# Performance work log

Measured on AMD Instinct MI355X. Metric: run time of the kernel, lower is better.

The kernel has to match this reference:

```python
import jax, jax.numpy as jnp
import numpy as np

B, N, D = 64, 128, 512
NEG = 1e30


def _gru_cell(x, h, Wi, Wh, bi, bh):
    # torch nn.GRUCell math
    gi = x @ Wi.T + bi  # (B, 3D)
    gh = h @ Wh.T + bh  # (B, 3D)
    ir, iz, inn = jnp.split(gi, 3, axis=-1)
    hr, hz, hn = jnp.split(gh, 3, axis=-1)
    r = jax.nn.sigmoid(ir + hr)
    z = jax.nn.sigmoid(iz + hz)
    n = jnp.tanh(inn + r * hn)
    return (1.0 - z) * n + z * h


def setup_inputs() -> dict:
    key = jax.random.key(0)
    ks = jax.random.split(key, 16)
    s = 1.0 / np.sqrt(D)
    u = lambda k, shape: jax.random.uniform(k, shape, jnp.float32, -s, s)
    adj = jax.random.randint(ks[13], (B, N, N), 0, 2, jnp.int32)
    adj = adj.at[:, :, 0].set(1)  # ensure each causal prefix has >=1 unmasked edge
    s_mask = jax.random.randint(ks[14], (B, N, N), 0, 2, jnp.int32)
    o_mask = 1 - s_mask
    return {
        "features": jax.random.normal(ks[0], (B, N, D), jnp.float32),
        "Wi_c": u(ks[1], (3 * D, D)),
        "Wh_c": u(ks[2], (3 * D, D)),
        "bi_c": u(ks[3], (3 * D,)),
        "bh_c": u(ks[4], (3 * D,)),
        "Wi_p": u(ks[5], (3 * D, D)),
        "Wh_p": u(ks[6], (3 * D, D)),
        "bi_p": u(ks[7], (3 * D,)),
        "bh_p": u(ks[8], (3 * D,)),
        "lin_w": u(ks[9], (1, 2 * D)),
        "lin_b": u(ks[10], (1,)),
        "Wr0": u(ks[11], (D, D)),
        "Wr1": u(ks[12], (D, D)),
        "adj": adj,
        "s_mask": s_mask,
        "o_mask": o_mask,
    }


def reference(features, Wi_c, Wh_c, bi_c, bh_c, Wi_p, Wh_p, bi_p, bh_p,
              lin_w, lin_b, Wr0, Wr1, adj, s_mask, o_mask):
    dt = features.dtype
    adj_f = adj.astype(dt)
    s_f = s_mask.astype(dt)
    o_f = o_mask.astype(dt)
    wq = lin_w[0, :D]   # applies to Q half of cat(Q, K)
    wk = lin_w[0, D:]   # applies to K half
    b = lin_b[0]
    pos = jnp.arange(N)

    # step 0
    x0 = features[:, 0]
    zeros = jnp.zeros((B, D), dt)
    C0 = _gru_cell(x0, zeros, Wi_c, Wh_c, bi_c, bh_c)
    P0 = _gru_cell(zeros, x0, Wi_p, Wh_p, bi_p, bh_p)
    H0 = jnp.zeros((B, N, D), dt).at[:, 0].set(C0 + P0)

    def step(H, inputs):
        i, x, adj_row, s_row, o_row = inputs
        # masked graph attention over the causal prefix [0, i)
        alpha = (x @ wq)[:, None] + H @ wk + b          # (B, N)
        valid = adj_row * (pos < i).astype(dt)          # (B, N)
        alpha = alpha - (1.0 - valid) * NEG
        w = jax.nn.softmax(alpha, axis=1)               # (B, N)
        V = (H @ Wr0.T) * s_row[:, :, None] + (H @ Wr1.T) * o_row[:, :, None]
        M = jnp.einsum('bn,bnd->bd', w, V)              # (B, D)
        C = _gru_cell(x, M, Wi_c, Wh_c, bi_c, bh_c)
        P = _gru_cell(M, x, Wi_p, Wh_p, bi_p, bh_p)
        H = H.at[:, i].set(C + P)
        return H, None

    xs = (jnp.arange(1, N),
          jnp.swapaxes(features, 0, 1)[1:],
          jnp.swapaxes(adj_f, 0, 1)[1:],
          jnp.swapaxes(s_f, 0, 1)[1:],
          jnp.swapaxes(o_f, 0, 1)[1:])
    H1, _ = jax.lax.scan(step, H0, xs)
    return H1
```

## Files before the change

kernel.cpp:

```cpp
#include <hip/hip_runtime.h>

#define BB 64
#define NN 128
#define DD 512
#define NBLK 128
#define NTHR 512
#define GCOLS 24
#define WCS 2056
#define WXS 1032
#define BCS 6656
#define UBE (BB * 2048)

typedef unsigned short u16;
typedef unsigned int u32;
typedef unsigned long long u64;
typedef __attribute__((ext_vector_type(8))) __bf16 bf16x8;
typedef __attribute__((ext_vector_type(4))) float f32x4;

#define MFMA16(a, b, c) __builtin_amdgcn_mfma_f32_16x16x32_bf16((a), (b), (c), 0, 0, 0)

__device__ __forceinline__ float b2f(u16 u) {
    union { u32 i; float f; } c; c.i = ((u32)u) << 16; return c.f;
}
__device__ __forceinline__ u16 f2b(float f) {
    union { float f; u32 i; } c; c.f = f;
    return (u16)((c.i + 0x7FFFu + ((c.i >> 16) & 1u)) >> 16);
}
__device__ __forceinline__ float sigm(float x) { return 1.f / (1.f + __expf(-x)); }
__device__ __forceinline__ float tanh_(float x) {
    x = fminf(fmaxf(x, -15.f), 15.f);
    float e = __expf(2.f * x);
    return (e - 1.f) / (e + 1.f);
}

__device__ __forceinline__ float ld_cohf(const float* p) {
    return __hip_atomic_load((float*)p, __ATOMIC_RELAXED, __HIP_MEMORY_SCOPE_AGENT);
}
__device__ __forceinline__ void st_cohf(float* p, float v) {
    __hip_atomic_store(p, v, __ATOMIC_RELAXED, __HIP_MEMORY_SCOPE_AGENT);
}
__device__ __forceinline__ void st_cohu32(u32* p, u32 v) {
    __hip_atomic_store(p, v, __ATOMIC_RELAXED, __HIP_MEMORY_SCOPE_AGENT);
}

template<bool CACHED>
__device__ __forceinline__ bf16x8 ldu16(const u16* p) {
    if constexpr (CACHED) {
        return *(const bf16x8*)p;
    } else {
        union { bf16x8 v; u64 q[2]; } u;
        u.q[0] = __hip_atomic_load((u64*)p,     __ATOMIC_RELAXED, __HIP_MEMORY_SCOPE_AGENT);
        u.q[1] = __hip_atomic_load((u64*)p + 1, __ATOMIC_RELAXED, __HIP_MEMORY_SCOPE_AGENT);
        return u.v;
    }
}

__device__ __forceinline__ void gbar(int* sync, int gen, int blk) {
    __syncthreads();
    int* epoch = sync;
    if (blk == 0) {
        const int t = threadIdx.x;
        int done = (t == 0 || t >= NBLK) ? 1 : 0;
        int* myarr = sync + 256 + t * 16;
        int it = 0;
        for (;;) {
            if (!done) {
                int v = ((it & 15) == 15)
                    ? __hip_atomic_load(myarr, __ATOMIC_ACQUIRE, __HIP_MEMORY_SCOPE_AGENT)
                    : __hip_atomic_load(myarr, __ATOMIC_RELAXED, __HIP_MEMORY_SCOPE_AGENT);
                done = (v >= gen);
            }
            ++it;
            if (__syncthreads_and(done)) break;
            __builtin_amdgcn_s_sleep(1);
        }
        if (t == 0) {
            (void)__hip_atomic_load(sync + 256 + 16, __ATOMIC_ACQUIRE, __HIP_MEMORY_SCOPE_AGENT);
            __hip_atomic_store(epoch, gen, __ATOMIC_RELEASE, __HIP_MEMORY_SCOPE_AGENT);
        }
        __syncthreads();
    } else {
        if (threadIdx.x == 0) {
            __hip_atomic_store(sync + 256 + blk * 16, gen, __ATOMIC_RELEASE, __HIP_MEMORY_SCOPE_AGENT);
            int it = 0;
            for (;;) {
                int v = ((it & 15) == 15)
                    ? __hip_atomic_load(epoch, __ATOMIC_ACQUIRE, __HIP_MEMORY_SCOPE_AGENT)
                    : __hip_atomic_load(epoch, __ATOMIC_RELAXED, __HIP_MEMORY_SCOPE_AGENT);
                ++it;
                if (v >= gen) break;
                __builtin_amdgcn_s_sleep(1);
            }
            (void)__hip_atomic_load(epoch, __ATOMIC_ACQUIRE, __HIP_MEMORY_SCOPE_AGENT);
        }
        __syncthreads();
    }
}

__device__ __forceinline__ void gbar_lite(int* flags, int gen, int blk,
                                          int nsig, bool sig, bool wait) {
    __syncthreads();
    if (sig && threadIdx.x == 0)
        __hip_atomic_store(flags + blk * 32, gen, __ATOMIC_RELAXED, __HIP_MEMORY_SCOPE_AGENT);
    if (wait) {
        const int t = threadIdx.x;
        int done = (t >= nsig) ? 1 : 0;
        int* f = flags + t * 32;
        for (;;) {
            if (!done) {
                int v = __hip_atomic_load(f, __ATOMIC_RELAXED, __HIP_MEMORY_SCOPE_AGENT);
                done = (v >= gen);
            }
            if (__syncthreads_and(done)) break;
            __builtin_amdgcn_s_sleep(2);
        }
    }
    asm volatile("" ::: "memory");
    __builtin_amdgcn_sched_barrier(0);
}

template<bool CACHED>
__device__ __forceinline__ void gates_merged(
    const u16* __restrict__ ub, const u16* s_wc, const float* s_gb,
    float* __restrict__ bc, int blk, int rt, int lr, int lq)
{
    const int cc0 = lr, cc1 = lr + 8;
    const u16* w0 = s_wc + cc0 * WCS;
    const u16* w1 = s_wc + cc1 * WCS;
    const u16* arow = ub + (size_t)(rt * 16 + lr) * 2048;
    f32x4 acc0 = {0.f, 0.f, 0.f, 0.f}, acc1 = {0.f, 0.f, 0.f, 0.f};
    #pragma unroll 4
    for (int c = 0; c < 16; ++c) {
        int kk = c * 32 + lq * 8;
        bf16x8 ah = ldu16<CACHED>(arow + kk);
        bf16x8 al = ldu16<CACHED>(arow + 512 + kk);
        bf16x8 wh0 = *(const bf16x8*)(w0 + kk);
        bf16x8 wl0 = *(const bf16x8*)(w0 + 1024 + kk);
        bf16x8 wh1 = *(const bf16x8*)(w1 + kk);
        bf16x8 wl1 = *(const bf16x8*)(w1 + 1024 + kk);
        acc0 = MFMA16(ah, wh0, acc0); acc0 = MFMA16(al, wh0, acc0); acc0 = MFMA16(ah, wl0, acc0);
        acc1 = MFMA16(ah, wh1, acc1); acc1 = MFMA16(al, wh1, acc1); acc1 = MFMA16(ah, wl1, acc1);
    }
    #pragma unroll 4
    for (int c = 0; c < 16; ++c) {
        int kk = c * 32 + lq * 8;
        bf16x8 ah = ldu16<CACHED>(arow + 1024 + kk);
        bf16x8 al = ldu16<CACHED>(arow + 1536 + kk);
        bf16x8 wh0 = *(const bf16x8*)(w0 + 512 + kk);
        bf16x8 wl0 = *(const bf16x8*)(w0 + 1536 + kk);
        bf16x8 wh1 = *(const bf16x8*)(w1 + 512 + kk);
        bf16x8 wl1 = *(const bf16x8*)(w1 + 1536 + kk);
        acc0 = MFMA16(ah, wh0, acc0); acc0 = MFMA16(al, wh0, acc0); acc0 = MFMA16(ah, wl0, acc0);
        acc1 = MFMA16(ah, wh1, acc1); acc1 = MFMA16(al, wh1, acc1); acc1 = MFMA16(ah, wl1, acc1);
    }
    float b0 = s_gb[cc0], b1 = s_gb[cc1];
    int col0 = blk * GCOLS + cc0, col1 = blk * GCOLS + cc1;
    #pragma unroll
    for (int r = 0; r < 4; ++r) {
        size_t row = (size_t)(rt * 16 + lq * 4 + r) * BCS;
        st_cohf(bc + row + 512 + col0, acc0[r] + b0);
        st_cohf(bc + row + 512 + col1, acc1[r] + b1);
    }
}

__device__ __forceinline__ void x_task(
    int i, const u16* __restrict__ featblob, const u16* s_wxw, const float* s_xb,
    float* __restrict__ bc, int blk, int task, int lr, int lq)
{
    const int ct = task & 1, rt = task >> 1;
    const int cc = ct * 8 + lr;
    const int col = blk * GCOLS + cc;
    const u16* wcol = s_wxw + cc * WXS;
    const u16* arow = featblob + (size_t)(i * 64 + rt * 16 + lr) * 1024;
    f32x4 acc = {0.f, 0.f, 0.f, 0.f};
    #pragma unroll 4
    for (int c = 0; c < 16; ++c) {
        int kk = c * 32 + lq * 8;
        bf16x8 ah = *(const bf16x8*)(arow + kk);
        bf16x8 al = *(const bf16x8*)(arow + 512 + kk);
        bf16x8 wh = *(const bf16x8*)(wcol + kk);
        bf16x8 wl = *(const bf16x8*)(wcol + 512 + kk);
        acc = MFMA16(ah, wh, acc); acc = MFMA16(al, wh, acc); acc = MFMA16(ah, wl, acc);
    }
    float bias = s_xb[cc];
    #pragma unroll
    for (int r = 0; r < 4; ++r)
        st_cohf(bc + (size_t)(rt * 16 + lq * 4 + r) * BCS + 3584 + col, acc[r] + bias);
}

template<bool CACHED>
__device__ __forceinline__ void m_task(
    const u16* __restrict__ ub, const u16* __restrict__ WrB,
    float* __restrict__ bc, int blk, int lr, int lq)
{
    const int ct = blk >> 2, rt = blk & 3;
    const int col = ct * 16 + lr;
    const u16* wcol = WrB + (size_t)col * 2048;
    const u16* arow = ub + (size_t)(rt * 16 + lr) * 2048;
    f32x4 acc = {0.f, 0.f, 0.f, 0.f};
    #pragma unroll 4
    for (int c = 0; c < 16; ++c) {
        int kk = c * 32 + lq * 8;
        bf16x8 a0h = ldu16<CACHED>(arow + kk);
        bf16x8 a0l = ldu16<CACHED>(arow + 512 + kk);
        bf16x8 a1h = ldu16<CACHED>(arow + 1024 + kk);
        bf16x8 a1l = ldu16<CACHED>(arow + 1536 + kk);
        bf16x8 w0h = *(const bf16x8*)(wcol + kk);
        bf16x8 w0l = *(const bf16x8*)(wcol + 512 + kk);
        bf16x8 w1h = *(const bf16x8*)(wcol + 1024 + kk);
        bf16x8 w1l = *(const bf16x8*)(wcol + 1536 + kk);
        acc = MFMA16(a0h, w0h, acc); acc = MFMA16(a0l, w0h, acc); acc = MFMA16(a0h, w0l, acc);
        acc = MFMA16(a1h, w1h, acc); acc = MFMA16(a1l, w1h, acc); acc = MFMA16(a1h, w1l, acc);
    }
    #pragma unroll
    for (int r = 0; r < 4; ++r)
        st_cohf(bc + (size_t)(rt * 16 + lq * 4 + r) * BCS + col, acc[r]);
}

template<bool CACHED>
__device__ __forceinline__ void phb(
    int i, const u16* __restrict__ ub, const u16* __restrict__ featblob,
    const u16* __restrict__ WrB, const u16* s_wc, const u16* s_wxw,
    const float* s_gb, const float* s_xb,
    float* __restrict__ bc, int blk, int wv, int lr, int lq)
{
    if (wv < 4) {
        gates_merged<CACHED>(ub, s_wc, s_gb, bc, blk, wv, lr, lq);
    } else if (wv == 4) {
        x_task(i, featblob, s_wxw, s_xb, bc, blk, 0, lr, lq);
        x_task(i, featblob, s_wxw, s_xb, bc, blk, 1, lr, lq);
        x_task(i, featblob, s_wxw, s_xb, bc, blk, 2, lr, lq);
    } else if (wv == 5) {
        x_task(i, featblob, s_wxw, s_xb, bc, blk, 3, lr, lq);
        x_task(i, featblob, s_wxw, s_xb, bc, blk, 4, lr, lq);
        x_task(i, featblob, s_wxw, s_xb, bc, blk, 5, lr, lq);
    } else if (wv == 6) {
        x_task(i, featblob, s_wxw, s_xb, bc, blk, 6, lr, lq);
        x_task(i, featblob, s_wxw, s_xb, bc, blk, 7, lr, lq);
    } else {
        m_task<CACHED>(ub, WrB, bc, blk, lr, lq);
    }
}

__global__ __launch_bounds__(NTHR) void grn_kernel(
    const float* __restrict__ feat, const float* __restrict__ Wi_c, const float* __restrict__ Wh_c,
    const float* __restrict__ bi_c, const float* __restrict__ bh_c,
    const float* __restrict__ Wi_p, const float* __restrict__ Wh_p,
    const float* __restrict__ bi_p, const float* __restrict__ bh_p,
    const float* __restrict__ lin_w, const float* __restrict__ lin_b,
    const float* __restrict__ Wr0, const float* __restrict__ Wr1,
    const int* __restrict__ adj, const int* __restrict__ smask,
    float* __restrict__ out,
    float* __restrict__ q, u16* __restrict__ ublob,
    u16* __restrict__ featblob, float* __restrict__ bc, u16* __restrict__ WrB,
    int* __restrict__ sync, int use_ring)
{
    const int t = threadIdx.x, blk = blockIdx.x;
    const int lane = t & 63, wv = t >> 6;
    const int lr = lane & 15, lq = lane >> 4;
    int gen = 0;
    int* lsync = sync + 4096;

    __shared__ u16 s_wc[GCOLS * WCS];
    __shared__ __align__(16) char s_wx_raw[GCOLS * WXS * 2];
    __shared__ float s_u0[DD];
    __shared__ float s_ut[DD];
    __shared__ float s_red[NTHR];
    __shared__ float s_hk[NN];
    __shared__ float s_q[NN];
    __shared__ float s_w[NN];
    __shared__ float s_ws[NN];
    __shared__ float s_gb[GCOLS];
    __shared__ float s_xb[GCOLS];

    u16* s_wxw = (u16*)s_wx_raw;
    float* s_wgf = (float*)s_wx_raw;

    const float wkreg = lin_w[DD + t];

    for (int rr = 0; rr < 64; ++rr) {
        int gr = blk * 64 + rr;
        int bb_ = gr >> 7, nn_ = gr & 127;
        float x = feat[(size_t)gr * DD + t];
        u16 h = f2b(x);
        u16* dst = featblob + (size_t)(nn_ * 64 + bb_) * 1024;
        dst[t] = h;
        dst[512 + t] = f2b(x - b2f(h));
    }
    for (int cc = 0; cc < 4; ++cc) {
        int c = blk * 4 + cc;
        float w0 = Wr0[(size_t)c * DD + t], w1 = Wr1[(size_t)c * DD + t];
        u16 h0 = f2b(w0), h1 = f2b(w1);
        u16* dst = WrB + (size_t)c * 2048;
        dst[t] = h0; dst[512 + t] = f2b(w0 - b2f(h0));
        dst[1024 + t] = h1; dst[1536 + t] = f2b(w1 - b2f(h1));
    }
    {
        float linb = lin_b[0];
        float wqf[8];
        #pragma unroll
        for (int jj = 0; jj < 8; ++jj) wqf[jj] = lin_w[lane * 8 + jj];
        for (int rr = 0; rr < 8; ++rr) {
            int row = blk * 64 + wv * 8 + rr;
            const float* fp = feat + (size_t)row * DD + lane * 8;
            float p = 0.f;
            #pragma unroll
            for (int jj = 0; jj < 8; ++jj) p += fp[jj] * wqf[jj];
            #pragma unroll
            for (int off = 32; off; off >>= 1) p += __shfl_down(p, off, 64);
            if (lane == 0) q[row] = p + linb;
        }
    }
    {
        int jg0 = blk * GCOLS;
        for (int cc = 0; cc < GCOLS; ++cc) {
            int jg = jg0 + cc;
            const float* src = (jg < 1536) ? (Wh_c + (size_t)jg * DD) : (Wi_p + (size_t)(jg - 1536) * DD);
            s_wgf[t * GCOLS + cc] = src[t];
        }
        if (t < GCOLS) {
            int jg = jg0 + t;
            s_gb[t] = (jg < 1536) ? bh_c[jg] : bi_p[jg - 1536];
            s_xb[t] = (jg < 1536) ? bi_c[jg] : bh_p[jg - 1536];
        }
    }
    __syncthreads();
    {
        float acc0[GCOLS], acc1[GCOLS];
        #pragma unroll
        for (int cc = 0; cc < GCOLS; ++cc) { acc0[cc] = 0.f; acc1[cc] = 0.f; }
        for (int j = 0; j < DD; ++j) {
            float wr0 = Wr0[(size_t)j * DD + t];
            float wr1 = Wr1[(size_t)j * DD + t];
            const float* g = s_wgf + j * GCOLS;
            #pragma unroll
            for (int cc = 0; cc < GCOLS; ++cc) {
                float gv = g[cc];
                acc0[cc] += wr0 * gv;
                acc1[cc] += wr1 * gv;
            }
        }
        __syncthreads();
        #pragma unroll
        for (int cc = 0; cc < GCOLS; ++cc) {
            u16 h0 = f2b(acc0[cc]);
            s_wc[cc * WCS + t] = h0;
            s_wc[cc * WCS + 1024 + t] = f2b(acc0[cc] - b2f(h0));
            u16 h1 = f2b(acc1[cc]);
            s_wc[cc * WCS + 512 + t] = h1;
            s_wc[cc * WCS + 1536 + t] = f2b(acc1[cc] - b2f(h1));
        }
    }
    {
        int jx0 = blk * GCOLS;
        for (int cc = 0; cc < GCOLS; ++cc) {
            int jx = jx0 + cc;
            const float* src = (jx < 1536) ? (Wi_c + (size_t)jx * DD) : (Wh_p + (size_t)(jx - 1536) * DD);
            float w = src[t];
            u16 h = f2b(w);
            s_wxw[cc * WXS + t] = h;
            s_wxw[cc * WXS + 512 + t] = f2b(w - b2f(h));
        }
    }
    gbar(sync, ++gen, blk);

    x_task(0, featblob, s_wxw, s_xb, bc, blk, wv, lr, lq);
    if (blk < BB && t < NN) s_q[t] = q[blk * NN + t];
    gbar(sync, ++gen, blk);

    if (blk < BB) {
        const float* bcb = bc + (size_t)blk * BCS;
        float ir = ld_cohf(bcb + 3584 + t), iz = ld_cohf(bcb + 4096 + t), inn = ld_cohf(bcb + 4608 + t);
        float r = sigm(ir + bh_c[t]), z = sigm(iz + bh_c[512 + t]);
        float C = (1.f - z) * tanh_(inn + r * bh_c[1024 + t]);
        float ghr = ld_cohf(bcb + 5120 + t), ghz = ld_cohf(bcb + 5632 + t), ghn = ld_cohf(bcb + 6144 + t);
        float r2 = sigm(bi_p[t] + ghr), z2 = sigm(bi_p[512 + t] + ghz);
        float n2 = tanh_(bi_p[1024 + t] + r2 * ghn);
        float x = feat[(size_t)(blk * NN) * DD + t];
        float P = (1.f - z2) * n2 + z2 * x;
        float Hv = C + P;
        out[(size_t)(blk * NN) * DD + t] = Hv;
        s_red[t] = Hv * wkreg;
        __syncthreads();
        if (wv == 0) {
            float p = 0.f;
            #pragma unroll
            for (int jj = 0; jj < 8; ++jj) p += s_red[lane + 64 * jj];
            #pragma unroll
            for (int off = 32; off; off >>= 1) p += __shfl_down(p, off, 64);
            if (lane == 0) s_hk[0] = p;
        }
    }
    gbar(sync, ++gen, blk);

    for (int i = 1; i < NN; ++i) {
        u16* ub_i = ublob + (size_t)(use_ring ? (NN - 1 - i) : 0) * UBE;

        if (blk < BB) {
            int va0 = 0, va1 = 0, vs0 = 0, vs1 = 0;
            float qv = 0.f;
            if (wv == 0) {
                const int* ar_ = adj + (size_t)(blk * NN + i) * NN;
                const int* sr_ = smask + (size_t)(blk * NN + i) * NN;
                va0 = ar_[lane]; va1 = ar_[lane + 64];
                vs0 = sr_[lane]; vs1 = sr_[lane + 64];
                qv = s_q[i];
            }
            if (i >= 2) {
                int j = i - 1;
                const float* bcb = bc + (size_t)blk * BCS;
                float Mv = ld_cohf(bcb + t);
                float hr = ld_cohf(bcb + 512 + t), hz = ld_cohf(bcb + 1024 + t), hn = ld_cohf(bcb + 1536 + t);
                float gir = ld_cohf(bcb + 2048 + t), giz = ld_cohf(bcb + 2560 + t), gin = ld_cohf(bcb + 3072 + t);
                float ir = ld_cohf(bcb + 3584 + t), iz = ld_cohf(bcb + 4096 + t), inn = ld_cohf(bcb + 4608 + t);
                float ghr = ld_cohf(bcb + 5120 + t), ghz = ld_cohf(bcb + 5632 + t), ghn = ld_cohf(bcb + 6144 + t);
                float x = feat[(size_t)(blk * NN + j) * DD + t];
                float r = sigm(ir + hr), z = sigm(iz + hz);
                float C = (1.f - z) * tanh_(inn + r * hn) + z * Mv;
                float r2 = sigm(gir + ghr), z2 = sigm(giz + ghz);
                float P = (1.f - z2) * tanh_(gin + r2 * ghn) + z2 * x;
                float Hv = C + P;
                out[(size_t)(blk * NN + j) * DD + t] = Hv;
                s_red[t] = Hv * wkreg;
            }
            s_u0[t] = 0.f; s_ut[t] = 0.f;
            __syncthreads();
            if (wv == 0) {
                if (i >= 2) {
                    float p = 0.f;
                    #pragma unroll
                    for (int jj = 0; jj < 8; ++jj) p += s_red[lane + 64 * jj];
                    #pragma unroll
                    for (int off = 32; off; off >>= 1) p += __shfl_down(p, off, 64);
                    if (lane == 0) s_hk[i - 1] = p;
                }
                int n2i = lane + 64;
                float a0 = (lane < i && va0 != 0) ? (qv + s_hk[lane]) : -1e30f;
                float a1 = (n2i < i && va1 != 0) ? (qv + s_hk[n2i]) : -1e30f;
                float m = fmaxf(a0, a1);
                #pragma unroll
                for (int off = 32; off; off >>= 1) m = fmaxf(m, __shfl_xor(m, off, 64));
                float e0 = (a0 > -1e29f) ? __expf(a0 - m) : 0.f;
                float e1 = (a1 > -1e29f) ? __expf(a1 - m) : 0.f;
                float ss = e0 + e1;
                #pragma unroll
                for (int off = 32; off; off >>= 1) ss += __shfl_xor(ss, off, 64);
                float inv = 1.f / ss;
                float w0 = e0 * inv, w1 = e1 * inv;
                s_w[lane] = w0; s_w[n2i] = w1;
                s_ws[lane] = w0 * (float)vs0;
                s_ws[n2i] = w1 * (float)vs1;
            }
            __syncthreads();
            {
                int g = t >> 7, dqb = (t & 127) * 4;
                const float* Hb = out + (size_t)blk * NN * DD + dqb;
                f32x4 u0 = {0.f, 0.f, 0.f, 0.f}, ut = {0.f, 0.f, 0.f, 0.f};
                int n = g;
                for (; n + 12 < i; n += 16) {
                    f32x4 h0 = *(const f32x4*)(Hb + (size_t)n * DD);
                    f32x4 h1 = *(const f32x4*)(Hb + (size_t)(n + 4) * DD);
                    f32x4 h2 = *(const f32x4*)(Hb + (size_t)(n + 8) * DD);
                    f32x4 h3 = *(const f32x4*)(Hb + (size_t)(n + 12) * DD);
                    u0 += s_ws[n] * h0 + s_ws[n + 4] * h1 + s_ws[n + 8] * h2 + s_ws[n + 12] * h3;
                    ut += s_w[n] * h0 + s_w[n + 4] * h1 + s_w[n + 8] * h2 + s_w[n + 12] * h3;
                }
                for (; n < i; n += 4) {
                    f32x4 h0 = *(const f32x4*)(Hb + (size_t)n * DD);
                    u0 += s_ws[n] * h0;
                    ut += s_w[n] * h0;
                }
                #pragma unroll
                for (int e = 0; e < 4; ++e) {
                    atomicAdd(&s_u0[dqb + e], u0[e]);
                    atomicAdd(&s_ut[dqb + e], ut[e]);
                }
            }
            __syncthreads();
            {
                int tt = t & 255, sel = t >> 8;
                float a0 = s_u0[2 * tt],          a1 = s_u0[2 * tt + 1];
                float b0_ = s_ut[2 * tt] - a0,    b1_ = s_ut[2 * tt + 1] - a1;
                float v0 = sel ? b0_ : a0,        v1 = sel ? b1_ : a1;
                u16 h0 = f2b(v0), h1 = f2b(v1);
                u16 l0 = f2b(v0 - b2f(h0)), l1 = f2b(v1 - b2f(h1));
                u32 hw = (u32)h0 | ((u32)h1 << 16);
                u32 lw = (u32)l0 | ((u32)l1 << 16);
                u32* ub32 = (u32*)(ub_i + (size_t)blk * 2048);
                int base = sel * 512;
                st_cohu32(ub32 + base + tt, hw);
                st_cohu32(ub32 + base + 256 + tt, lw);
            }
        }
        gbar_lite(lsync, ++gen, blk, 64, blk < BB, true);

        if (use_ring)
            phb<true>(i, ub_i, featblob, WrB, s_wc, s_wxw, s_gb, s_xb, bc, blk, wv, lr, lq);
        else
            phb<false>(i, ub_i, featblob, WrB, s_wc, s_wxw, s_gb, s_xb, bc, blk, wv, lr, lq);

        gbar_lite(lsync, ++gen, blk, 128, true, blk < BB);
    }

    if (blk < BB) {
        int j = NN - 1;
        const float* bcb = bc + (size_t)blk * BCS;
        float Mv = ld_cohf(bcb + t);
        float hr = ld_cohf(bcb + 512 + t), hz = ld_cohf(bcb + 1024 + t), hn = ld_cohf(bcb + 1536 + t);
        float gir = ld_cohf(bcb + 2048 + t), giz = ld_cohf(bcb + 2560 + t), gin = ld_cohf(bcb + 3072 + t);
        float ir = ld_cohf(bcb + 3584 + t), iz = ld_cohf(bcb + 4096 + t), inn = ld_cohf(bcb + 4608 + t);
        float ghr = ld_cohf(bcb + 5120 + t), ghz = ld_cohf(bcb + 5632 + t), ghn = ld_cohf(bcb + 6144 + t);
        float x = feat[(size_t)(blk * NN + j) * DD + t];
        float r = sigm(ir + hr), z = sigm(iz + hz);
        float C = (1.f - z) * tanh_(inn + r * hn) + z * Mv;
        float r2 = sigm(gir + ghr), z2 = sigm(giz + ghz);
        float P = (1.f - z2) * tanh_(gin + r2 * ghn) + z2 * x;
        out[(size_t)(blk * NN + j) * DD + t] = C + P;
    }
}

extern "C" void kernel_launch(void* const* d_in, const int* in_sizes, int n_in,
                              void* d_out, int out_size, void* d_ws, size_t ws_size,
                              hipStream_t stream) {
    (void)in_sizes; (void)n_in; (void)out_size;
    const float* feat = (const float*)d_in[0];
    const float* Wi_c = (const float*)d_in[1];
    const float* Wh_c = (const float*)d_in[2];
    const float* bi_c = (const float*)d_in[3];
    const float* bh_c = (const float*)d_in[4];
    const float* Wi_p = (const float*)d_in[5];
    const float* Wh_p = (const float*)d_in[6];
    const float* bi_p = (const float*)d_in[7];
    const float* bh_p = (const float*)d_in[8];
    const float* lin_w = (const float*)d_in[9];
    const float* lin_b = (const float*)d_in[10];
    const float* Wr0 = (const float*)d_in[11];
    const float* Wr1 = (const float*)d_in[12];
    const int* adj = (const int*)d_in[13];
    const int* smask = (const int*)d_in[14];
    float* out = (float*)d_out;

    char* ws = (char*)d_ws;
    size_t off = 0;
    int* sync_ = (int*)(ws + off);      off += 32768;
    float* q = (float*)(ws + off);      off += (size_t)BB * NN * 4;
    u16* featblob = (u16*)(ws + off);   off += (size_t)BB * NN * 1024 * 2;
    float* bc = (float*)(ws + off);     off += (size_t)BB * BCS * 4;
    u16* WrB = (u16*)(ws + off);        off += (size_t)512 * 2048 * 2;
    u16* ublob = (u16*)(ws + off);
    size_t ring_bytes = (size_t)(NN - 1) * UBE * 2;
    int use_ring = (ws_size >= off + ring_bytes) ? 1 : 0;

    (void)hipMemsetAsync(d_ws, 0, 32768, stream);
    hipLaunchKernelGGL(grn_kernel, dim3(NBLK), dim3(NTHR), 0, stream,
                       feat, Wi_c, Wh_c, bi_c, bh_c, Wi_p, Wh_p, bi_p, bh_p,
                       lin_w, lin_b, Wr0, Wr1, adj, smask, out,
                       q, ublob, featblob, bc, WrB, sync_, use_ring);
}
```

Before: 4.142 ms.

## Precompute input-side GRU gates for all steps and replace barriers with per-group flags

The input-side GRU matmuls (x@Wi_c and x@Wh_p), which depend only on features, are computed for all steps up front into a workspace buffer. This removes them from the serial per-step critical path. The first per-step grid barrier becomes per-row-group flags that each gate and M wave polls before reading the shared u vector, so waves can start as soon as their 16 rows are ready. The atomic shared reduction is replaced by per-group partial sums added afterwards. The cost is a large extra workspace buffer (used only if ws_size allows) and a longer prologue.

Measured after the change: 3.517 ms. 15.1% less time.

```diff
diff --git a/kernel.cpp b/kernel.cpp
--- a/kernel.cpp
+++ b/kernel.cpp
@@ -41,6 +41,12 @@
 }
 __device__ __forceinline__ void st_cohu32(u32* p, u32 v) {
     __hip_atomic_store(p, v, __ATOMIC_RELAXED, __HIP_MEMORY_SCOPE_AGENT);
+}
+__device__ __forceinline__ void st_cohi(int* p, int v) {
+    __hip_atomic_store(p, v, __ATOMIC_RELAXED, __HIP_MEMORY_SCOPE_AGENT);
+}
+__device__ __forceinline__ int ld_cohi(int* p) {
+    return __hip_atomic_load(p, __ATOMIC_RELAXED, __HIP_MEMORY_SCOPE_AGENT);
 }
 
 template<bool CACHED>
@@ -101,19 +107,28 @@
                                           int nsig, bool sig, bool wait) {
     __syncthreads();
     if (sig && threadIdx.x == 0)
-        __hip_atomic_store(flags + blk * 32, gen, __ATOMIC_RELAXED, __HIP_MEMORY_SCOPE_AGENT);
+        st_cohi(flags + blk * 32, gen);
     if (wait) {
         const int t = threadIdx.x;
         int done = (t >= nsig) ? 1 : 0;
         int* f = flags + t * 32;
         for (;;) {
-            if (!done) {
-                int v = __hip_atomic_load(f, __ATOMIC_RELAXED, __HIP_MEMORY_SCOPE_AGENT);
-                done = (v >= gen);
-            }
+            if (!done) done = (ld_cohi(f) >= gen);
             if (__syncthreads_and(done)) break;
             __builtin_amdgcn_s_sleep(2);
         }
+    }
+    asm volatile("" ::: "memory");
+    __builtin_amdgcn_sched_barrier(0);
+}
+
+__device__ __forceinline__ void waitA(int* flagsA, int gen, int grp) {
+    const int l = threadIdx.x & 63;
+    int* f = flagsA + (grp * 16 + (l & 15)) * 32;
+    for (;;) {
+        int v = ld_cohi(f);
+        if (__all(v >= gen)) break;
+        __builtin_amdgcn_s_sleep(1);
     }
     asm volatile("" ::: "memory");
     __builtin_amdgcn_sched_barrier(0);
@@ -163,13 +178,13 @@
     }
 }
 
-__device__ __forceinline__ void x_task(
-    int i, const u16* __restrict__ featblob, const u16* s_wxw, const float* s_xb,
-    float* __restrict__ bc, int blk, int task, int lr, int lq)
+__device__ __forceinline__ f32x4 x_core(
+    int i, const u16* __restrict__ featblob, const u16* s_wxw,
+    int task, int lr, int lq, int* ccO)
 {
     const int ct = task & 1, rt = task >> 1;
     const int cc = ct * 8 + lr;
-    const int col = blk * GCOLS + cc;
+    *ccO = cc;
     const u16* wcol = s_wxw + cc * WXS;
     const u16* arow = featblob + (size_t)(i * 64 + rt * 16 + lr) * 1024;
     f32x4 acc = {0.f, 0.f, 0.f, 0.f};
@@ -182,10 +197,33 @@
         bf16x8 wl = *(const bf16x8*)(wcol + 512 + kk);
         acc = MFMA16(ah, wh, acc); acc = MFMA16(al, wh, acc); acc = MFMA16(ah, wl, acc);
     }
+    return acc;
+}
+
+__device__ __forceinline__ void x_task(
+    int i, const u16* __restrict__ featblob, const u16* s_wxw, const float* s_xb,
+    float* __restrict__ bc, int blk, int task, int lr, int lq)
+{
+    int cc; f32x4 acc = x_core(i, featblob, s_wxw, task, lr, lq, &cc);
+    const int rt = task >> 1;
+    const int col = blk * GCOLS + cc;
     float bias = s_xb[cc];
     #pragma unroll
     for (int r = 0; r < 4; ++r)
         st_cohf(bc + (size_t)(rt * 16 + lq * 4 + r) * BCS + 3584 + col, acc[r] + bias);
+}
+
+__device__ __forceinline__ void x_task_xg(
+    int i, const u16* __restrict__ featblob, const u16* s_wxw, const float* s_xb,
+    float* __restrict__ xg, int blk, int task, int lr, int lq)
+{
+    int cc; f32x4 acc = x_core(i, featblob, s_wxw, task, lr, lq, &cc);
+    const int rt = task >> 1;
+    const int col = blk * GCOLS + cc;
+    float bias = s_xb[cc];
+    #pragma unroll
+    for (int r = 0; r < 4; ++r)
+        xg[((size_t)i * 64 + rt * 16 + lq * 4 + r) * 3072 + col] = acc[r] + bias;
 }
 
 template<bool CACHED>
@@ -217,31 +255,6 @@
         st_cohf(bc + (size_t)(rt * 16 + lq * 4 + r) * BCS + col, acc[r]);
 }
 
-template<bool CACHED>
-__device__ __forceinline__ void phb(
-    int i, const u16* __restrict__ ub, const u16* __restrict__ featblob,
-    const u16* __restrict__ WrB, const u16* s_wc, const u16* s_wxw,
-    const float* s_gb, const float* s_xb,
-    float* __restrict__ bc, int blk, int wv, int lr, int lq)
-{
-    if (wv < 4) {
-        gates_merged<CACHED>(ub, s_wc, s_gb, bc, blk, wv, lr, lq);
-    } else if (wv == 4) {
-        x_task(i, featblob, s_wxw, s_xb, bc, blk, 0, lr, lq);
-        x_task(i, featblob, s_wxw, s_xb, bc, blk, 1, lr, lq);
-        x_task(i, featblob, s_wxw, s_xb, bc, blk, 2, lr, lq);
-    } else if (wv == 5) {
-        x_task(i, featblob, s_wxw, s_xb, bc, blk, 3, lr, lq);
-        x_task(i, featblob, s_wxw, s_xb, bc, blk, 4, lr, lq);
-        x_task(i, featblob, s_wxw, s_xb, bc, blk, 5, lr, lq);
-    } else if (wv == 6) {
-        x_task(i, featblob, s_wxw, s_xb, bc, blk, 6, lr, lq);
-        x_task(i, featblob, s_wxw, s_xb, bc, blk, 7, lr, lq);
-    } else {
-        m_task<CACHED>(ub, WrB, bc, blk, lr, lq);
-    }
-}
-
 __global__ __launch_bounds__(NTHR) void grn_kernel(
     const float* __restrict__ feat, const float* __restrict__ Wi_c, const float* __restrict__ Wh_c,
     const float* __restrict__ bi_c, const float* __restrict__ bh_c,
@@ -253,13 +266,14 @@
     float* __restrict__ out,
     float* __restrict__ q, u16* __restrict__ ublob,
     u16* __restrict__ featblob, float* __restrict__ bc, u16* __restrict__ WrB,
-    int* __restrict__ sync, int use_ring)
+    float* __restrict__ xg, int* __restrict__ sync, int use_ring, int use_xg)
 {
     const int t = threadIdx.x, blk = blockIdx.x;
     const int lane = t & 63, wv = t >> 6;
     const int lr = lane & 15, lq = lane >> 4;
     int gen = 0;
-    int* lsync = sync + 4096;
+    int* flagsA = sync + 4096;
+    int* flagsB = sync + 8192;
 
     __shared__ u16 s_wc[GCOLS * WCS];
     __shared__ __align__(16) char s_wx_raw[GCOLS * WXS * 2];
@@ -275,6 +289,7 @@
 
     u16* s_wxw = (u16*)s_wx_raw;
     float* s_wgf = (float*)s_wx_raw;
+    float* s_part = (float*)s_wx_raw;
 
     const float wkreg = lin_w[DD + t];
 
@@ -365,6 +380,10 @@
     gbar(sync, ++gen, blk);
 
     x_task(0, featblob, s_wxw, s_xb, bc, blk, wv, lr, lq);
+    if (use_xg) {
+        for (int ii = 0; ii < NN; ++ii)
+            x_task_xg(ii, featblob, s_wxw, s_xb, xg, blk, wv, lr, lq);
+    }
     if (blk < BB && t < NN) s_q[t] = q[blk * NN + t];
     gbar(sync, ++gen, blk);
 
@@ -412,8 +431,15 @@
                 float Mv = ld_cohf(bcb + t);
                 float hr = ld_cohf(bcb + 512 + t), hz = ld_cohf(bcb + 1024 + t), hn = ld_cohf(bcb + 1536 + t);
                 float gir = ld_cohf(bcb + 2048 + t), giz = ld_cohf(bcb + 2560 + t), gin = ld_cohf(bcb + 3072 + t);
-                float ir = ld_cohf(bcb + 3584 + t), iz = ld_cohf(bcb + 4096 + t), inn = ld_cohf(bcb + 4608 + t);
-                float ghr = ld_cohf(bcb + 5120 + t), ghz = ld_cohf(bcb + 5632 + t), ghn = ld_cohf(bcb + 6144 + t);
+                float ir, iz, inn, ghr, ghz, ghn;
+                if (use_xg) {
+                    const float* xrow = xg + ((size_t)j * 64 + blk) * 3072;
+                    ir = xrow[t]; iz = xrow[512 + t]; inn = xrow[1024 + t];
+                    ghr = xrow[1536 + t]; ghz = xrow[2048 + t]; ghn = xrow[2560 + t];
+                } else {
+                    ir = ld_cohf(bcb + 3584 + t); iz = ld_cohf(bcb + 4096 + t); inn = ld_cohf(bcb + 4608 + t);
+                    ghr = ld_cohf(bcb + 5120 + t); ghz = ld_cohf(bcb + 5632 + t); ghn = ld_cohf(bcb + 6144 + t);
+                }
                 float x = feat[(size_t)(blk * NN + j) * DD + t];
                 float r = sigm(ir + hr), z = sigm(iz + hz);
                 float C = (1.f - z) * tanh_(inn + r * hn) + z * Mv;
@@ -423,7 +449,7 @@
                 out[(size_t)(blk * NN + j) * DD + t] = Hv;
                 s_red[t] = Hv * wkreg;
             }
-            s_u0[t] = 0.f; s_ut[t] = 0.f;
+            if (!use_xg) { s_u0[t] = 0.f; s_ut[t] = 0.f; }
             __syncthreads();
             if (wv == 0) {
                 if (i >= 2) {
@@ -470,18 +496,37 @@
                     u0 += s_ws[n] * h0;
                     ut += s_w[n] * h0;
                 }
-                #pragma unroll
-                for (int e = 0; e < 4; ++e) {
-                    atomicAdd(&s_u0[dqb + e], u0[e]);
-                    atomicAdd(&s_ut[dqb + e], ut[e]);
+                if (use_xg) {
+                    float* spg = s_part + g * 1024;
+                    *(f32x4*)&spg[dqb] = u0;
+                    *(f32x4*)&spg[512 + dqb] = ut;
+                } else {
+                    #pragma unroll
+                    for (int e = 0; e < 4; ++e) {
+                        atomicAdd(&s_u0[dqb + e], u0[e]);
+                        atomicAdd(&s_ut[dqb + e], ut[e]);
+                    }
                 }
             }
             __syncthreads();
             {
                 int tt = t & 255, sel = t >> 8;
-                float a0 = s_u0[2 * tt],          a1 = s_u0[2 * tt + 1];
-                float b0_ = s_ut[2 * tt] - a0,    b1_ = s_ut[2 * tt + 1] - a1;
-                float v0 = sel ? b0_ : a0,        v1 = sel ? b1_ : a1;
+                float a0, a1, t0_, t1_;
+                if (use_xg) {
+                    a0 = s_part[2 * tt]            + s_part[1024 + 2 * tt]
+                       + s_part[2048 + 2 * tt]     + s_part[3072 + 2 * tt];
+                    a1 = s_part[2 * tt + 1]        + s_part[1024 + 2 * tt + 1]
+                       + s_part[2048 + 2 * tt + 1] + s_part[3072 + 2 * tt + 1];
+                    t0_ = s_part[512 + 2 * tt]        + s_part[1536 + 2 * tt]
+                        + s_part[2560 + 2 * tt]       + s_part[3584 + 2 * tt];
+                    t1_ = s_part[512 + 2 * tt + 1]    + s_part[1536 + 2 * tt + 1]
+                        + s_part[2560 + 2 * tt + 1]   + s_part[3584 + 2 * tt + 1];
+                } else {
+                    a0 = s_u0[2 * tt]; a1 = s_u0[2 * tt + 1];
+                    t0_ = s_ut[2 * tt]; t1_ = s_ut[2 * tt + 1];
+                }
+                float b0_ = t0_ - a0, b1_ = t1_ - a1;
+                float v0 = sel ? b0_ : a0, v1 = sel ? b1_ : a1;
                 u16 h0 = f2b(v0), h1 = f2b(v1);
                 u16 l0 = f2b(v0 - b2f(h0)), l1 = f2b(v1 - b2f(h1));
                 u32 hw = (u32)h0 | ((u32)h1 << 16);
@@ -491,15 +536,42 @@
                 st_cohu32(ub32 + base + tt, hw);
                 st_cohu32(ub32 + base + 256 + tt, lw);
             }
-        }
-        gbar_lite(lsync, ++gen, blk, 64, blk < BB, true);
-
-        if (use_ring)
-            phb<true>(i, ub_i, featblob, WrB, s_wc, s_wxw, s_gb, s_xb, bc, blk, wv, lr, lq);
-        else
-            phb<false>(i, ub_i, featblob, WrB, s_wc, s_wxw, s_gb, s_xb, bc, blk, wv, lr, lq);
-
-        gbar_lite(lsync, ++gen, blk, 128, true, blk < BB);
+            __syncthreads();
+            if (t == 0) st_cohi(flagsA + blk * 32, i);
+        }
+
+        if (use_xg) {
+            if (wv < 4) {
+                waitA(flagsA, i, wv);
+                if (use_ring) gates_merged<true >(ub_i, s_wc, s_gb, bc, blk, wv, lr, lq);
+                else          gates_merged<false>(ub_i, s_wc, s_gb, bc, blk, wv, lr, lq);
+            } else if (wv == 7) {
+                waitA(flagsA, i, blk & 3);
+                if (use_ring) m_task<true >(ub_i, WrB, bc, blk, lr, lq);
+                else          m_task<false>(ub_i, WrB, bc, blk, lr, lq);
+            }
+        } else {
+            if (wv < 4) {
+                waitA(flagsA, i, wv);
+                gates_merged<false>(ub_i, s_wc, s_gb, bc, blk, wv, lr, lq);
+            } else if (wv == 4) {
+                x_task(i, featblob, s_wxw, s_xb, bc, blk, 0, lr, lq);
+                x_task(i, featblob, s_wxw, s_xb, bc, blk, 1, lr, lq);
+                x_task(i, featblob, s_wxw, s_xb, bc, blk, 2, lr, lq);
+            } else if (wv == 5) {
+                x_task(i, featblob, s_wxw, s_xb, bc, blk, 3, lr, lq);
+                x_task(i, featblob, s_wxw, s_xb, bc, blk, 4, lr, lq);
+                x_task(i, featblob, s_wxw, s_xb, bc, blk, 5, lr, lq);
+            } else if (wv == 6) {
+                x_task(i, featblob, s_wxw, s_xb, bc, blk, 6, lr, lq);
+                x_task(i, featblob, s_wxw, s_xb, bc, blk, 7, lr, lq);
+            } else {
+                waitA(flagsA, i, blk & 3);
+                m_task<false>(ub_i, WrB, bc, blk, lr, lq);
+            }
+        }
+
+        gbar_lite(flagsB, i, blk, NBLK, true, blk < BB);
     }
 
     if (blk < BB) {
@@ -508,8 +580,15 @@
         float Mv = ld_cohf(bcb + t);
         float hr = ld_cohf(bcb + 512 + t), hz = ld_cohf(bcb + 1024 + t), hn = ld_cohf(bcb + 1536 + t);
         float gir = ld_cohf(bcb + 2048 + t), giz = ld_cohf(bcb + 2560 + t), gin = ld_cohf(bcb + 3072 + t);
-        float ir = ld_cohf(bcb + 3584 + t), iz = ld_cohf(bcb + 4096 + t), inn = ld_cohf(bcb + 4608 + t);
-        float ghr = ld_cohf(bcb + 5120 + t), ghz = ld_cohf(bcb + 5632 + t), ghn = ld_cohf(bcb + 6144 + t);
+        float ir, iz, inn, ghr, ghz, ghn;
+        if (use_xg) {
+            const float* xrow = xg + ((size_t)j * 64 + blk) * 3072;
+            ir = xrow[t]; iz = xrow[512 + t]; inn = xrow[1024 + t];
+            ghr = xrow[1536 + t]; ghz = xrow[2048 + t]; ghn = xrow[2560 + t];
+        } else {
+            ir = ld_cohf(bcb + 3584 + t); iz = ld_cohf(bcb + 4096 + t); inn = ld_cohf(bcb + 4608 + t);
+            ghr = ld_cohf(bcb + 5120 + t); ghz = ld_cohf(bcb + 5632 + t); ghn = ld_cohf(bcb + 6144 + t);
+        }
         float x = feat[(size_t)(blk * NN + j) * DD + t];
         float r = sigm(ir + hr), z = sigm(iz + hz);
         float C = (1.f - z) * tanh_(inn + r * hn) + z * Mv;
@@ -542,18 +621,21 @@
 
     char* ws = (char*)d_ws;
     size_t off = 0;
-    int* sync_ = (int*)(ws + off);      off += 32768;
+    int* sync_ = (int*)(ws + off);      off += 65536;
     float* q = (float*)(ws + off);      off += (size_t)BB * NN * 4;
     u16* featblob = (u16*)(ws + off);   off += (size_t)BB * NN * 1024 * 2;
     float* bc = (float*)(ws + off);     off += (size_t)BB * BCS * 4;
     u16* WrB = (u16*)(ws + off);        off += (size_t)512 * 2048 * 2;
     u16* ublob = (u16*)(ws + off);
     size_t ring_bytes = (size_t)(NN - 1) * UBE * 2;
+    size_t xg_bytes = (size_t)NN * 64 * 3072 * 4;
     int use_ring = (ws_size >= off + ring_bytes) ? 1 : 0;
-
-    (void)hipMemsetAsync(d_ws, 0, 32768, stream);
+    float* xg = (float*)(ws + off + ring_bytes);
+    int use_xg = (use_ring && ws_size >= off + ring_bytes + xg_bytes) ? 1 : 0;
+
+    (void)hipMemsetAsync(d_ws, 0, 65536, stream);
     hipLaunchKernelGGL(grn_kernel, dim3(NBLK), dim3(NTHR), 0, stream,
                        feat, Wi_c, Wh_c, bi_c, bh_c, Wi_p, Wh_p, bi_p, bh_p,
                        lin_w, lin_b, Wr0, Wr1, adj, smask, out,
-                       q, ublob, featblob, bc, WrB, sync_, use_ring);
-}
+                       q, ublob, featblob, bc, WrB, xg, sync_, use_ring, use_xg);
+}
```
